# Kernel tuning notes

Measured on AMD Instinct MI355X. Metric: run time of the kernel, lower is better.

Reference implementation:

```python
import jax, jax.numpy as jnp
import numpy as np

BS, C, N = 2, 128, 4096
EPS = 1e-5  # BatchNorm eps (eval mode, fresh running stats: mean=0, var=1)


def conv1x1(x, W, b):
    # Conv1d kernel_size=1 == per-position linear: x [b,cin,n], W [cout,cin]
    return jnp.einsum('oc,bcn->bon', W, x) + b[None, :, None]


def bn_eval(x, gamma, beta):
    # eval-mode BatchNorm1d with running_mean=0, running_var=1
    s = gamma / jnp.sqrt(1.0 + EPS)
    return x * s[None, :, None] + beta[None, :, None]


def setup_inputs() -> dict:
    key = jax.random.key(0)
    ks = jax.random.split(key, 16)
    sc = 1.0 / np.sqrt(C)
    h = C // 2
    return {
        'feat': jax.random.normal(ks[0], (BS, C, N), jnp.float32),
        'attention': jax.random.uniform(ks[1], (BS, N, N), jnp.float32),
        'Wq': jax.random.normal(ks[2], (C, C), jnp.float32) * sc,
        'bq': jnp.zeros((C,), jnp.float32),
        'Wk': jax.random.normal(ks[3], (C, C), jnp.float32) * sc,
        'bk': jnp.zeros((C,), jnp.float32),
        'Wv': jax.random.normal(ks[4], (C, C), jnp.float32) * sc,
        'bv': jnp.zeros((C,), jnp.float32),
        'W1': jax.random.normal(ks[5], (h, C), jnp.float32) * sc,
        'b1': jnp.zeros((h,), jnp.float32),
        'g1': jnp.ones((h,), jnp.float32),
        'be1': jnp.zeros((h,), jnp.float32),
        'W2': jax.random.normal(ks[6], (h, h), jnp.float32) * (1.0 / np.sqrt(h)),
        'b2': jnp.zeros((h,), jnp.float32),
        'g2': jnp.ones((h,), jnp.float32),
        'be2': jnp.zeros((h,), jnp.float32),
        'W3': jax.random.normal(ks[7], (C, h), jnp.float32) * (1.0 / np.sqrt(h)),
        'b3': jnp.zeros((C,), jnp.float32),
        'H': jax.random.randint(ks[8], (BS, N, N), 0, 2).astype(jnp.float32),
    }


def reference(feat, attention, Wq, bq, Wk, bk, Wv, bv,
              W1, b1, g1, be1, W2, b2, g2, be2, W3, b3, H):
    # projections (single head: head dim == C)
    Q = conv1x1(feat, Wq, bq)  # [b,C,N]
    K = conv1x1(feat, Wk, bk)
    V = conv1x1(feat, Wv, bv)
    # scores [b,N,N]: einsum('bhco,bhci->bhoi') with h=1
    scores = jnp.einsum('bco,bci->boi', Q, K) / np.sqrt(C)
    # additive mask: (1-H) -> -1e9 where complement is nonzero
    mask = jnp.where(H < 0.5, -1e9, 0.0)
    weight = jax.nn.softmax(attention * scores + mask, axis=-1)  # [b,N,N]
    message = jnp.einsum('boi,bci->bco', weight, V)  # [b,C,N]
    # fc_message: conv-bn-relu x2 -> conv
    m = jax.nn.relu(bn_eval(conv1x1(message, W1, b1), g1, be1))
    m = jax.nn.relu(bn_eval(conv1x1(m, W2, b2), g2, be2))
    m = conv1x1(m, W3, b3)
    return feat + m
```

## Files before the change

### kernel.cpp

```cpp
#include <hip/hip_runtime.h>
#include <stdint.h>

typedef __attribute__((ext_vector_type(8))) short bf16x8;
typedef __attribute__((ext_vector_type(4))) float f32x4;
typedef __attribute__((ext_vector_type(4))) unsigned short us4;

#define NPOS 4096
#define CD 128

__device__ __forceinline__ float b2f(unsigned short u) {
  union { float f; uint32_t i; } x; x.i = ((uint32_t)u) << 16; return x.f;
}
__device__ __forceinline__ unsigned short f2b(float f) {
  union { float f; uint32_t i; } x; x.f = f;
  uint32_t r = x.i + 0x7FFFu + ((x.i >> 16) & 1u);
  return (unsigned short)(r >> 16);
}

#define WQ_O 0
#define WK_O 16384
#define WV_O 32768
#define W1_O 49152
#define W2_O 57344
#define W3_O 61440
#define BQ_O 69632
#define BK_O 69760
#define BV_O 69888
#define B1_O 70016
#define G1_O 70080
#define BE1_O 70144
#define B2_O 70208
#define G2_O 70272
#define BE2_O 70336
#define B3_O 70400
#define WB_ELEMS 70656

__global__ __launch_bounds__(64) void probe_kernel(const unsigned short* __restrict__ att_u16,
                                                   int* __restrict__ flag) {
  int lane = threadIdx.x;
  float mx = 0.f;
  for (int k = lane; k < 4096; k += 64) {
    float v = fabsf(b2f(att_u16[2 * k]));
    if (v > mx && v == v) mx = v;
  }
  unsigned long long b = __ballot(mx > 100.f);
  if (lane == 0) *flag = (b != 0ull) ? 1 : 0;
}

__device__ __forceinline__ void cvt_range(const void* src, unsigned short* dst, int n,
                                          bool f32, int tid, int nthreads) {
  if (f32) {
    const float* s = (const float*)src;
    for (int i = tid; i < n; i += nthreads) dst[i] = f2b(s[i]);
  } else {
    const unsigned short* s = (const unsigned short*)src;
    for (int i = tid; i < n; i += nthreads) dst[i] = s[i];
  }
}

__global__ __launch_bounds__(256) void prep_kernel(
    const int* __restrict__ flag, const void* feat,
    const void* Wq, const void* bq, const void* Wk, const void* bk,
    const void* Wv, const void* bv, const void* W1, const void* b1,
    const void* g1, const void* be1, const void* W2, const void* b2,
    const void* g2, const void* be2, const void* W3, const void* b3,
    unsigned short* __restrict__ featb, unsigned short* __restrict__ wb) {
  bool f32 = (*flag != 0);
  int tid = blockIdx.x * 256 + threadIdx.x;
  int nt = gridDim.x * 256;
  cvt_range(feat, featb, 2 * CD * NPOS, f32, tid, nt);
  cvt_range(Wq, wb + WQ_O, 16384, f32, tid, nt);
  cvt_range(Wk, wb + WK_O, 16384, f32, tid, nt);
  cvt_range(Wv, wb + WV_O, 16384, f32, tid, nt);
  cvt_range(W1, wb + W1_O, 8192, f32, tid, nt);
  cvt_range(W2, wb + W2_O, 4096, f32, tid, nt);
  cvt_range(W3, wb + W3_O, 8192, f32, tid, nt);
  cvt_range(bq, wb + BQ_O, 128, f32, tid, nt);
  cvt_range(bk, wb + BK_O, 128, f32, tid, nt);
  cvt_range(bv, wb + BV_O, 128, f32, tid, nt);
  cvt_range(b1, wb + B1_O, 64, f32, tid, nt);
  cvt_range(g1, wb + G1_O, 64, f32, tid, nt);
  cvt_range(be1, wb + BE1_O, 64, f32, tid, nt);
  cvt_range(b2, wb + B2_O, 64, f32, tid, nt);
  cvt_range(g2, wb + G2_O, 64, f32, tid, nt);
  cvt_range(be2, wb + BE2_O, 64, f32, tid, nt);
  cvt_range(b3, wb + B3_O, 128, f32, tid, nt);
}

__global__ __launch_bounds__(256) void qkv_kernel(
    const unsigned short* __restrict__ featb, const unsigned short* __restrict__ wb,
    unsigned short* __restrict__ QT, unsigned short* __restrict__ KT,
    unsigned short* __restrict__ Vm) {
  __shared__ __attribute__((aligned(16))) unsigned short X[128][136];
  int tid = threadIdx.x;
  int w = tid >> 6, lane = tid & 63;
  int hi = lane >> 4, lo = lane & 15;
  int n0 = blockIdx.x * 128;
  int proj = blockIdx.y;
  int bat = blockIdx.z;
  const unsigned short* W = wb + (proj == 0 ? WQ_O : (proj == 1 ? WK_O : WV_O));
  const unsigned short* bias = wb + (proj == 0 ? BQ_O : (proj == 1 ? BK_O : BV_O));

  #pragma unroll
  for (int it = 0; it < 8; ++it) {
    int row = it * 16 + (tid >> 4);
    int col = (tid & 15) * 8;
    *(bf16x8*)&X[row][col] =
        *(const bf16x8*)(featb + ((size_t)(bat * CD + row)) * NPOS + n0 + col);
  }
  __syncthreads();

  int wr = w >> 1, wc = w & 1;
  f32x4 acc[4][4];
  #pragma unroll
  for (int m = 0; m < 4; ++m)
    #pragma unroll
    for (int n = 0; n < 4; ++n) acc[m][n] = (f32x4){0.f, 0.f, 0.f, 0.f};

  #pragma unroll
  for (int ks = 0; ks < 4; ++ks) {
    int c0 = ks * 32 + 8 * hi;
    bf16x8 a[4], bb[4];
    #pragma unroll
    for (int m = 0; m < 4; ++m) {
      int o = wr * 64 + m * 16 + lo;
      a[m] = *(const bf16x8*)(W + o * CD + c0);
    }
    #pragma unroll
    for (int n = 0; n < 4; ++n) {
      int nn = wc * 64 + n * 16 + lo;
      bf16x8 t;
      #pragma unroll
      for (int e = 0; e < 8; ++e) t[e] = (short)X[c0 + e][nn];
      bb[n] = t;
    }
    #pragma unroll
    for (int m = 0; m < 4; ++m)
      #pragma unroll
      for (int n = 0; n < 4; ++n)
        acc[m][n] = __builtin_amdgcn_mfma_f32_16x16x32_bf16(a[m], bb[n], acc[m][n], 0, 0, 0);
  }

  #pragma unroll
  for (int m = 0; m < 4; ++m) {
    int o0 = wr * 64 + m * 16 + hi * 4;
    float bsv[4];
    #pragma unroll
    for (int r = 0; r < 4; ++r) bsv[r] = b2f(bias[o0 + r]);
    #pragma unroll
    for (int n = 0; n < 4; ++n) {
      int nn = n0 + wc * 64 + n * 16 + lo;
      if (proj < 2) {
        unsigned short* O = proj == 0 ? QT : KT;
        us4 pk;
        #pragma unroll
        for (int r = 0; r < 4; ++r) pk[r] = f2b(acc[m][n][r] + bsv[r]);
        *(us4*)(O + ((size_t)(bat * NPOS + nn)) * CD + o0) = pk;
      } else {
        #pragma unroll
        for (int r = 0; r < 4; ++r)
          Vm[((size_t)(bat * CD + o0 + r)) * NPOS + nn] = f2b(acc[m][n][r] + bsv[r]);
      }
    }
  }
}

__global__ __launch_bounds__(512, 1) void attn_kernel(
    const int* __restrict__ flag,
    const unsigned short* __restrict__ QT, const unsigned short* __restrict__ KT,
    const unsigned short* __restrict__ Vm, const void* __restrict__ att,
    const void* __restrict__ Hm, unsigned short* __restrict__ MT) {
  __shared__ __attribute__((aligned(16))) unsigned short Pl[8][32][72];
  __shared__ float mred[8][32], lred[8][32];
  __shared__ float Olds[32][132];

  bool f32 = (*flag != 0);
  const float* attf = (const float*)att;
  const float* hmf = (const float*)Hm;
  const unsigned short* attu = (const unsigned short*)att;
  const unsigned short* hmu = (const unsigned short*)Hm;

  int tid = threadIdx.x;
  int w = tid >> 6, lane = tid & 63;
  int hi = lane >> 4, lo = lane & 15;
  int ob = blockIdx.x * 32;
  int bat = blockIdx.y;
  const float SCL = 0.088388347648318447f;

  bf16x8 qf[2][4];
  #pragma unroll
  for (int cf = 0; cf < 2; ++cf)
    #pragma unroll
    for (int ks = 0; ks < 4; ++ks)
      qf[cf][ks] = *(const bf16x8*)(QT + ((size_t)(bat * NPOS + ob + cf * 16 + lo)) * CD +
                                    ks * 32 + 8 * hi);

  f32x4 oacc[2][8];
  #pragma unroll
  for (int rp = 0; rp < 2; ++rp)
    #pragma unroll
    for (int c8 = 0; c8 < 8; ++c8) oacc[rp][c8] = (f32x4){0.f, 0.f, 0.f, 0.f};
  float mrun[2], lrun[2];
  #pragma unroll
  for (int cf = 0; cf < 2; ++cf) { mrun[cf] = -1e30f; lrun[cf] = 0.f; }

  for (int it = 0; it < 8; ++it) {
    int i0w = it * 512 + w * 64;

    us4 av[2][4], hv[2][4];
    #pragma unroll
    for (int cf = 0; cf < 2; ++cf)
      #pragma unroll
      for (int rf = 0; rf < 4; ++rf) {
        size_t idx = ((size_t)(bat * NPOS + ob + cf * 16 + lo)) * NPOS +
                     i0w + rf * 16 + 4 * hi;
        if (f32) {
          us4 a, h;
          #pragma unroll
          for (int rr = 0; rr < 4; ++rr) {
            a[rr] = f2b(attf[idx + rr]);
            h[rr] = f2b(hmf[idx + rr]);
          }
          av[cf][rf] = a; hv[cf][rf] = h;
        } else {
          av[cf][rf] = *(const us4*)(attu + idx);
          hv[cf][rf] = *(const us4*)(hmu + idx);
        }
      }

    f32x4 s2[4][2];
    #pragma unroll
    for (int rf = 0; rf < 4; ++rf)
      #pragma unroll
      for (int cf = 0; cf < 2; ++cf) s2[rf][cf] = (f32x4){0.f, 0.f, 0.f, 0.f};
    #pragma unroll
    for (int ks = 0; ks < 4; ++ks) {
      bf16x8 kf[4];
      #pragma unroll
      for (int rf = 0; rf < 4; ++rf)
        kf[rf] = *(const bf16x8*)(KT + ((size_t)(bat * NPOS + i0w + rf * 16 + lo)) * CD +
                                  ks * 32 + 8 * hi);
      #pragma unroll
      for (int rf = 0; rf < 4; ++rf) {
        s2[rf][0] = __builtin_amdgcn_mfma_f32_16x16x32_bf16(kf[rf], qf[0][ks], s2[rf][0], 0, 0, 0);
        s2[rf][1] = __builtin_amdgcn_mfma_f32_16x16x32_bf16(kf[rf], qf[1][ks], s2[rf][1], 0, 0, 0);
      }
    }

    float lg[2][4][4], mx[2];
    #pragma unroll
    for (int cf = 0; cf < 2; ++cf) {
      float m = -1e30f;
      #pragma unroll
      for (int rf = 0; rf < 4; ++rf)
        #pragma unroll
        for (int rr = 0; rr < 4; ++rr) {
          float a = b2f(av[cf][rf][rr]);
          bool msk = b2f(hv[cf][rf][rr]) < 0.5f;
          float v = msk ? -1e9f : a * SCL * s2[rf][cf][rr];
          lg[cf][rf][rr] = v;
          m = fmaxf(m, v);
        }
      m = fmaxf(m, __shfl_xor(m, 16, 64));
      m = fmaxf(m, __shfl_xor(m, 32, 64));
      mx[cf] = m;
    }

    float psc[2];
    #pragma unroll
    for (int cf = 0; cf < 2; ++cf) {
      float mo = mrun[cf];
      float mn = fmaxf(mo, mx[cf]);
      psc[cf] = __expf(mo - mn);
      mrun[cf] = mn;
    }

    #pragma unroll
    for (int cf = 0; cf < 2; ++cf) {
      float t = 0.f;
      #pragma unroll
      for (int rf = 0; rf < 4; ++rf) {
        us4 pk;
        #pragma unroll
        for (int rr = 0; rr < 4; ++rr) {
          float p = __expf(lg[cf][rf][rr] - mrun[cf]);
          t += p;
          pk[rr] = f2b(p);
        }
        *(us4*)&Pl[w][cf * 16 + lo][rf * 16 + 4 * hi] = pk;
      }
      t += __shfl_xor(t, 16, 64);
      t += __shfl_xor(t, 32, 64);
      lrun[cf] = lrun[cf] * psc[cf] + t;
    }

    #pragma unroll
    for (int rp = 0; rp < 2; ++rp) {
      #pragma unroll
      for (int rr = 0; rr < 4; ++rr) {
        float sc = __shfl(psc[rp], 4 * hi + rr, 64);
        #pragma unroll
        for (int c8 = 0; c8 < 8; ++c8) oacc[rp][c8][rr] *= sc;
      }
    }

    bf16x8 pa[2][2];
    #pragma unroll
    for (int rp = 0; rp < 2; ++rp)
      #pragma unroll
      for (int ks = 0; ks < 2; ++ks)
        pa[rp][ks] = *(const bf16x8*)&Pl[w][rp * 16 + lo][ks * 32 + 8 * hi];
    #pragma unroll
    for (int ks = 0; ks < 2; ++ks)
      #pragma unroll
      for (int c8 = 0; c8 < 8; ++c8) {
        bf16x8 bb = *(const bf16x8*)(Vm + ((size_t)(bat * CD + c8 * 16 + lo)) * NPOS +
                                     i0w + ks * 32 + 8 * hi);
        oacc[0][c8] = __builtin_amdgcn_mfma_f32_16x16x32_bf16(pa[0][ks], bb, oacc[0][c8], 0, 0, 0);
        oacc[1][c8] = __builtin_amdgcn_mfma_f32_16x16x32_bf16(pa[1][ks], bb, oacc[1][c8], 0, 0, 0);
      }
  }

  #pragma unroll
  for (int cf = 0; cf < 2; ++cf)
    if (hi == 0) { mred[w][cf * 16 + lo] = mrun[cf]; lred[w][cf * 16 + lo] = lrun[cf]; }
  __syncthreads();

  #pragma unroll
  for (int rp = 0; rp < 2; ++rp) {
    #pragma unroll
    for (int rr = 0; rr < 4; ++rr) {
      int o = rp * 16 + 4 * hi + rr;
      float ms = mred[0][o];
      #pragma unroll
      for (int v = 1; v < 8; ++v) ms = fmaxf(ms, mred[v][o]);
      float mw = __shfl(mrun[rp], 4 * hi + rr, 64);
      float fs = __expf(mw - ms);
      #pragma unroll
      for (int c8 = 0; c8 < 8; ++c8) oacc[rp][c8][rr] *= fs;
    }
  }

  for (int v = 0; v < 8; ++v) {
    if (w == v) {
      #pragma unroll
      for (int rp = 0; rp < 2; ++rp)
        #pragma unroll
        for (int c8 = 0; c8 < 8; ++c8)
          #pragma unroll
          for (int rr = 0; rr < 4; ++rr) {
            int row = rp * 16 + 4 * hi + rr, col = c8 * 16 + lo;
            if (v == 0) Olds[row][col] = oacc[rp][c8][rr];
            else Olds[row][col] += oacc[rp][c8][rr];
          }
    }
    __syncthreads();
  }

  {
    int row = tid >> 4, c0 = (tid & 15) * 8;
    float ms = mred[0][row];
    #pragma unroll
    for (int v = 1; v < 8; ++v) ms = fmaxf(ms, mred[v][row]);
    float L = 0.f;
    #pragma unroll
    for (int v = 0; v < 8; ++v) L += lred[v][row] * __expf(mred[v][row] - ms);
    float inv = 1.f / fmaxf(L, 1e-30f);
    bf16x8 p1;
    #pragma unroll
    for (int j = 0; j < 8; ++j) p1[j] = (short)f2b(Olds[row][c0 + j] * inv);
    *(bf16x8*)(MT + ((size_t)(bat * NPOS + ob + row)) * CD + c0) = p1;
  }
}

__global__ __launch_bounds__(256) void mlp_kernel(
    const int* __restrict__ flag,
    const unsigned short* __restrict__ MT, const unsigned short* __restrict__ featb,
    const unsigned short* __restrict__ wb, void* __restrict__ out) {
  __shared__ __attribute__((aligned(16))) unsigned short M1T[128][72];
  __shared__ __attribute__((aligned(16))) unsigned short M2T[128][72];
  __shared__ __attribute__((aligned(16))) unsigned short OT[128][136];
  __shared__ float A1[64], B1[64], A2[64], B2[64], BI3[128];

  bool f32 = (*flag != 0);
  int tid = threadIdx.x;
  int w = tid >> 6, lane = tid & 63;
  int hi = lane >> 4, lo = lane & 15;
  int n0 = blockIdx.x * 128;
  int bat = blockIdx.y;

  float rs = rsqrtf(1.0f + 1e-5f);
  if (tid < 64) {
    float s1 = b2f(wb[G1_O + tid]) * rs;
    A1[tid] = s1; B1[tid] = s1 * b2f(wb[B1_O + tid]) + b2f(wb[BE1_O + tid]);
    float s2 = b2f(wb[G2_O + tid]) * rs;
    A2[tid] = s2; B2[tid] = s2 * b2f(wb[B2_O + tid]) + b2f(wb[BE2_O + tid]);
  }
  if (tid < 128) BI3[tid] = b2f(wb[B3_O + tid]);
  __syncthreads();

  f32x4 acc1[4][2];
  #pragma unroll
  for (int m = 0; m < 4; ++m)
    #pragma unroll
    for (int n = 0; n < 2; ++n) acc1[m][n] = (f32x4){0.f, 0.f, 0.f, 0.f};
  #pragma unroll
  for (int ks = 0; ks < 4; ++ks) {
    bf16x8 bw[2];
    #pragma unroll
    for (int n = 0; n < 2; ++n)
      bw[n] = *(const bf16x8*)(MT + ((size_t)(bat * NPOS + n0 + w * 32 + n * 16 + lo)) * CD +
                               ks * 32 + 8 * hi);
    #pragma unroll
    for (int m = 0; m < 4; ++m) {
      bf16x8 aw = *(const bf16x8*)(wb + W1_O + (m * 16 + lo) * CD + ks * 32 + 8 * hi);
      #pragma unroll
      for (int n = 0; n < 2; ++n)
        acc1[m][n] = __builtin_amdgcn_mfma_f32_16x16x32_bf16(aw, bw[n], acc1[m][n], 0, 0, 0);
    }
  }
  #pragma unroll
  for (int m = 0; m < 4; ++m)
    #pragma unroll
    for (int n = 0; n < 2; ++n) {
      int h0 = m * 16 + hi * 4;
      int nn = w * 32 + n * 16 + lo;
      us4 pk;
      #pragma unroll
      for (int r = 0; r < 4; ++r) {
        float v = A1[h0 + r] * acc1[m][n][r] + B1[h0 + r];
        pk[r] = f2b(fmaxf(v, 0.f));
      }
      *(us4*)&M1T[nn][h0] = pk;
    }

  f32x4 acc2[4][2];
  #pragma unroll
  for (int m = 0; m < 4; ++m)
    #pragma unroll
    for (int n = 0; n < 2; ++n) acc2[m][n] = (f32x4){0.f, 0.f, 0.f, 0.f};
  #pragma unroll
  for (int ks = 0; ks < 2; ++ks) {
    bf16x8 bw[2];
    #pragma unroll
    for (int n = 0; n < 2; ++n)
      bw[n] = *(const bf16x8*)&M1T[w * 32 + n * 16 + lo][ks * 32 + 8 * hi];
    #pragma unroll
    for (int m = 0; m < 4; ++m) {
      bf16x8 aw = *(const bf16x8*)(wb + W2_O + (m * 16 + lo) * 64 + ks * 32 + 8 * hi);
      #pragma unroll
      for (int n = 0; n < 2; ++n)
        acc2[m][n] = __builtin_amdgcn_mfma_f32_16x16x32_bf16(aw, bw[n], acc2[m][n], 0, 0, 0);
    }
  }
  #pragma unroll
  for (int m = 0; m < 4; ++m)
    #pragma unroll
    for (int n = 0; n < 2; ++n) {
      int h0 = m * 16 + hi * 4;
      int nn = w * 32 + n * 16 + lo;
      us4 pk;
      #pragma unroll
      for (int r = 0; r < 4; ++r) {
        float v = A2[h0 + r] * acc2[m][n][r] + B2[h0 + r];
        pk[r] = f2b(fmaxf(v, 0.f));
      }
      *(us4*)&M2T[nn][h0] = pk;
    }

  f32x4 acc3[8][2];
  #pragma unroll
  for (int m = 0; m < 8; ++m)
    #pragma unroll
    for (int n = 0; n < 2; ++n) acc3[m][n] = (f32x4){0.f, 0.f, 0.f, 0.f};
  #pragma unroll
  for (int ks = 0; ks < 2; ++ks) {
    bf16x8 bw[2];
    #pragma unroll
    for (int n = 0; n < 2; ++n)
      bw[n] = *(const bf16x8*)&M2T[w * 32 + n * 16 + lo][ks * 32 + 8 * hi];
    #pragma unroll
    for (int m = 0; m < 8; ++m) {
      bf16x8 aw = *(const bf16x8*)(wb + W3_O + (m * 16 + lo) * 64 + ks * 32 + 8 * hi);
      #pragma unroll
      for (int n = 0; n < 2; ++n)
        acc3[m][n] = __builtin_amdgcn_mfma_f32_16x16x32_bf16(aw, bw[n], acc3[m][n], 0, 0, 0);
    }
  }
  #pragma unroll
  for (int m = 0; m < 8; ++m)
    #pragma unroll
    for (int n = 0; n < 2; ++n)
      #pragma unroll
      for (int r = 0; r < 4; ++r) {
        int c = m * 16 + hi * 4 + r;
        int nn = w * 32 + n * 16 + lo;
        OT[c][nn] = f2b(acc3[m][n][r] + BI3[c]);
      }
  __syncthreads();

  {
    int c = tid >> 1, nb = (tid & 1) * 64;
    #pragma unroll
    for (int j = 0; j < 8; ++j) {
      bf16x8 mv = *(bf16x8*)&OT[c][nb + 8 * j];
      const unsigned short* fp = featb + ((size_t)(bat * CD + c)) * NPOS + n0 + nb + 8 * j;
      bf16x8 fv = *(const bf16x8*)fp;
      float vals[8];
      #pragma unroll
      for (int e = 0; e < 8; ++e)
        vals[e] = b2f((unsigned short)mv[e]) + b2f((unsigned short)fv[e]);
      size_t oidx = ((size_t)(bat * CD + c)) * NPOS + n0 + nb + 8 * j;
      if (f32) {
        float* of = (float*)out;
        f32x4 v0 = {vals[0], vals[1], vals[2], vals[3]};
        f32x4 v1 = {vals[4], vals[5], vals[6], vals[7]};
        *(f32x4*)(of + oidx) = v0;
        *(f32x4*)(of + oidx + 4) = v1;
      } else {
        unsigned short* ou = (unsigned short*)out;
        bf16x8 ov;
        #pragma unroll
        for (int e = 0; e < 8; ++e) ov[e] = (short)f2b(vals[e]);
        *(bf16x8*)(ou + oidx) = ov;
      }
    }
  }
}

extern "C" void kernel_launch(void* const* d_in, const int* in_sizes, int n_in,
                              void* d_out, int out_size, void* d_ws, size_t ws_size,
                              hipStream_t stream) {
  const void* feat = d_in[0];
  const void* att  = d_in[1];
  const void* Wq = d_in[2];  const void* bq = d_in[3];
  const void* Wk = d_in[4];  const void* bk = d_in[5];
  const void* Wv = d_in[6];  const void* bv = d_in[7];
  const void* W1 = d_in[8];  const void* b1 = d_in[9];
  const void* g1 = d_in[10]; const void* be1 = d_in[11];
  const void* W2 = d_in[12]; const void* b2 = d_in[13];
  const void* g2 = d_in[14]; const void* be2 = d_in[15];
  const void* W3 = d_in[16]; const void* b3 = d_in[17];
  const void* Hm = d_in[18];

  int* flag = (int*)d_ws;
  unsigned short* base = (unsigned short*)((char*)d_ws + 256);
  unsigned short* featb = base;
  unsigned short* wb = featb + (size_t)2 * CD * NPOS;
  unsigned short* QT = wb + WB_ELEMS;
  unsigned short* KT = QT + (size_t)2 * NPOS * CD;
  unsigned short* Vm = KT + (size_t)2 * NPOS * CD;
  unsigned short* MT = Vm + (size_t)2 * NPOS * CD;

  hipLaunchKernelGGL(probe_kernel, dim3(1), dim3(64), 0, stream,
                     (const unsigned short*)att, flag);
  hipLaunchKernelGGL(prep_kernel, dim3(256), dim3(256), 0, stream,
                     flag, feat, Wq, bq, Wk, bk, Wv, bv, W1, b1, g1, be1,
                     W2, b2, g2, be2, W3, b3, featb, wb);
  hipLaunchKernelGGL(qkv_kernel, dim3(32, 3, 2), dim3(256), 0, stream,
                     featb, wb, QT, KT, Vm);
  hipLaunchKernelGGL(attn_kernel, dim3(128, 2), dim3(512), 0, stream,
                     flag, QT, KT, Vm, att, Hm, MT);
  hipLaunchKernelGGL(mlp_kernel, dim3(32, 2), dim3(256), 0, stream,
                     flag, MT, featb, wb, d_out);
}
```

Baseline: 167.5 us.

## Split attention key range across two blocks and merge partial softmax results

Splits the key dimension of the attention kernel into two halves along a new grid z dimension. Each half writes unnormalized partial outputs plus running max and sum to workspace, and a new merge kernel combines them with log-sum-exp rescaling. The grid goes from 256 to 512 blocks so more CUs on the device get work. The cost is an extra kernel launch and fp32 partial traffic, and it falls back to the old path if the workspace is too small.

```diff
diff --git a/kernel.cpp b/kernel.cpp
--- a/kernel.cpp
+++ b/kernel.cpp
@@ -169,7 +169,8 @@
     const int* __restrict__ flag,
     const unsigned short* __restrict__ QT, const unsigned short* __restrict__ KT,
     const unsigned short* __restrict__ Vm, const void* __restrict__ att,
-    const void* __restrict__ Hm, unsigned short* __restrict__ MT) {
+    const void* __restrict__ Hm, unsigned short* __restrict__ MT,
+    float* __restrict__ PO, float* __restrict__ ML, int niter, int partial) {
   __shared__ __attribute__((aligned(16))) unsigned short Pl[8][32][72];
   __shared__ float mred[8][32], lred[8][32];
   __shared__ float Olds[32][132];
@@ -185,6 +186,8 @@
   int hi = lane >> 4, lo = lane & 15;
   int ob = blockIdx.x * 32;
   int bat = blockIdx.y;
+  int half = blockIdx.z;
+  int ibase = half * niter * 512;
   const float SCL = 0.088388347648318447f;
 
   bf16x8 qf[2][4];
@@ -204,8 +207,8 @@
   #pragma unroll
   for (int cf = 0; cf < 2; ++cf) { mrun[cf] = -1e30f; lrun[cf] = 0.f; }
 
-  for (int it = 0; it < 8; ++it) {
-    int i0w = it * 512 + w * 64;
+  for (int it = 0; it < niter; ++it) {
+    int i0w = ibase + it * 512 + w * 64;
 
     us4 av[2][4], hv[2][4];
     #pragma unroll
@@ -217,10 +220,7 @@
         if (f32) {
           us4 a, h;
           #pragma unroll
-          for (int rr = 0; rr < 4; ++rr) {
-            a[rr] = f2b(attf[idx + rr]);
-            h[rr] = f2b(hmf[idx + rr]);
-          }
+          for (int rr = 0; rr < 4; ++rr) { a[rr] = f2b(attf[idx + rr]); h[rr] = f2b(hmf[idx + rr]); }
           av[cf][rf] = a; hv[cf][rf] = h;
         } else {
           av[cf][rf] = *(const us4*)(attu + idx);
@@ -365,12 +365,47 @@
     float L = 0.f;
     #pragma unroll
     for (int v = 0; v < 8; ++v) L += lred[v][row] * __expf(mred[v][row] - ms);
-    float inv = 1.f / fmaxf(L, 1e-30f);
-    bf16x8 p1;
-    #pragma unroll
-    for (int j = 0; j < 8; ++j) p1[j] = (short)f2b(Olds[row][c0 + j] * inv);
-    *(bf16x8*)(MT + ((size_t)(bat * NPOS + ob + row)) * CD + c0) = p1;
-  }
+
+    if (partial) {
+      size_t pidx = ((size_t)((bat * 128 + blockIdx.x) * 2 + half) * 32 + row) * 128 + c0;
+      #pragma unroll
+      for (int j = 0; j < 8; ++j) PO[pidx + j] = Olds[row][c0 + j];
+      if ((tid & 15) == 0) {
+        size_t midx = (size_t)((bat * 128 + blockIdx.x) * 2 + half) * 64 + row;
+        ML[midx] = ms;
+        ML[midx + 32] = L;
+      }
+    } else {
+      float inv = 1.f / fmaxf(L, 1e-30f);
+      bf16x8 p1;
+      #pragma unroll
+      for (int j = 0; j < 8; ++j) p1[j] = (short)f2b(Olds[row][c0 + j] * inv);
+      *(bf16x8*)(MT + ((size_t)(bat * NPOS + ob + row)) * CD + c0) = p1;
+    }
+  }
+}
+
+__global__ __launch_bounds__(512) void merge_kernel(
+    const float* __restrict__ PO, const float* __restrict__ ML,
+    unsigned short* __restrict__ MT) {
+  int tid = threadIdx.x;
+  int row = tid >> 4, c0 = (tid & 15) * 8;
+  int ot = blockIdx.x, bat = blockIdx.y;
+  size_t idx0 = (size_t)((bat * 128 + ot) * 2 + 0);
+  size_t idx1 = idx0 + 1;
+  float m0 = ML[idx0 * 64 + row], l0 = ML[idx0 * 64 + 32 + row];
+  float m1 = ML[idx1 * 64 + row], l1 = ML[idx1 * 64 + 32 + row];
+  float M = fmaxf(m0, m1);
+  float w0 = __expf(m0 - M), w1 = __expf(m1 - M);
+  float L = l0 * w0 + l1 * w1;
+  float inv = 1.f / fmaxf(L, 1e-30f);
+  size_t p0 = (idx0 * 32 + row) * 128 + c0;
+  size_t p1 = (idx1 * 32 + row) * 128 + c0;
+  bf16x8 out;
+  #pragma unroll
+  for (int j = 0; j < 8; ++j)
+    out[j] = (short)f2b((PO[p0 + j] * w0 + PO[p1 + j] * w1) * inv);
+  *(bf16x8*)(MT + ((size_t)(bat * NPOS + ot * 32 + row)) * CD + c0) = out;
 }
 
 __global__ __launch_bounds__(256) void mlp_kernel(
@@ -551,6 +586,11 @@
   unsigned short* KT = QT + (size_t)2 * NPOS * CD;
   unsigned short* Vm = KT + (size_t)2 * NPOS * CD;
   unsigned short* MT = Vm + (size_t)2 * NPOS * CD;
+  float* PO = (float*)(MT + (size_t)2 * NPOS * CD);
+  float* ML = PO + (size_t)512 * 32 * 128;
+
+  size_t need = ((char*)(ML + 512 * 64) - (char*)d_ws);
+  int use_split = (ws_size >= need) ? 1 : 0;
 
   hipLaunchKernelGGL(probe_kernel, dim3(1), dim3(64), 0, stream,
                      (const unsigned short*)att, flag);
@@ -559,8 +599,15 @@
                      W2, b2, g2, be2, W3, b3, featb, wb);
   hipLaunchKernelGGL(qkv_kernel, dim3(32, 3, 2), dim3(256), 0, stream,
                      featb, wb, QT, KT, Vm);
-  hipLaunchKernelGGL(attn_kernel, dim3(128, 2), dim3(512), 0, stream,
-                     flag, QT, KT, Vm, att, Hm, MT);
+  if (use_split) {
+    hipLaunchKernelGGL(attn_kernel, dim3(128, 2, 2), dim3(512), 0, stream,
+                       flag, QT, KT, Vm, att, Hm, MT, PO, ML, 4, 1);
+    hipLaunchKernelGGL(merge_kernel, dim3(128, 2), dim3(512), 0, stream,
+                       PO, ML, MT);
+  } else {
+    hipLaunchKernelGGL(attn_kernel, dim3(128, 2, 1), dim3(512), 0, stream,
+                       flag, QT, KT, Vm, att, Hm, MT, PO, ML, 8, 0);
+  }
   hipLaunchKernelGGL(mlp_kernel, dim3(32, 2), dim3(256), 0, stream,
                      flag, MT, featb, wb, d_out);
 }
```

New measurement: 180.8 us. 1.08x slower.
